# Optimization experiments

Measured on AMD Instinct MI355X. Metric: run time of the kernel, lower is better.

Reference implementation:

```python
import jax, jax.numpy as jnp
import numpy as np

B = 16; C = 20; M = 64
LEVELS = [("p3", 8, 128), ("p4", 16, 64), ("p5", 32, 32)]  # name, stride, H(=W)
BOUNDS = {"p3": (0.0, 64.0), "p4": (64.0, 128.0), "p5": (128.0, jnp.inf)}
TOPK = 1000; MAX_DET = 100; IOU_THR = 0.5; SCORE_THR = 0.3


def _grid(h, w, stride):
    # replicates get_fpn_location_coords (incl. torch's meshgrid(y, x) ordering)
    xs = stride * (jnp.arange(w, dtype=jnp.float32) + 0.5)
    ys = stride * (jnp.arange(h, dtype=jnp.float32) + 0.5)
    a, b = jnp.meshgrid(ys, xs, indexing="ij")
    return jnp.stack([a, b], axis=-1).reshape(h * w, 2)


def setup_inputs() -> dict:
    key = jax.random.key(0)
    ks = jax.random.split(key, 16)
    inp = {}
    inp["locs_p3"] = _grid(128, 128, 8)
    inp["locs_p4"] = _grid(64, 64, 16)
    inp["locs_p5"] = _grid(32, 32, 32)
    xy = jax.random.uniform(ks[0], (B, M, 2), minval=0.0, maxval=700.0)
    wh = jax.random.uniform(ks[1], (B, M, 2), minval=32.0, maxval=300.0)
    cid = jax.random.randint(ks[2], (B, M, 1), 0, C).astype(jnp.float32)
    gt = jnp.concatenate([xy, xy + wh, cid], axis=-1)
    pad = jnp.arange(M) >= (M - 16)  # last 16 rows are background padding
    inp["gt_boxes"] = jnp.where(pad[None, :, None], -1.0, gt)
    for i, (name, stride, h) in enumerate(LEVELS):
        n = h * h
        inp[f"cls_{name}"] = jax.random.normal(ks[3 + i], (B, n, C)) - 2.0
        inp[f"reg_{name}"] = jax.random.uniform(ks[6 + i], (B, n, 4), minval=0.0, maxval=8.0)
        inp[f"ctr_{name}"] = jax.random.normal(ks[9 + i], (B, n))
    return inp


def _match_level(centers, gt, lower, upper):
    # centers (N,2), gt (M,5) -> matched gt box per center (N,5), -1 for background
    x = centers[:, 0:1]; y = centers[:, 1:2]
    x0, y0, x1, y1 = gt[:, 0], gt[:, 1], gt[:, 2], gt[:, 3]
    ltrb = jnp.stack([x - x0[None], y - y0[None], x1[None] - x, y1[None] - y], axis=-1)  # (N,M,4)
    inside = ltrb.min(-1) > 0
    maxd = ltrb.max(-1)
    ok = inside & (maxd > lower) & (maxd < upper)
    areas = (x1 - x0) * (y1 - y0)
    quality = ok.astype(jnp.float32) * (1e8 - areas)[None, :]
    q = quality.max(-1)
    idx = jnp.argmax(quality, axis=-1)
    idx = jnp.where(q < 1e-5, -1, idx)
    matched = gt[jnp.clip(idx, 0)]
    return jnp.where((idx < 0)[:, None], -1.0, matched)


def _targets(centers, matched, stride):
    # fcos_get_deltas_from_locations + fcos_make_centerness_targets
    xc, yc = centers[:, 0], centers[:, 1]
    d = jnp.stack([(xc - matched[:, 0]) / stride, (yc - matched[:, 1]) / stride,
                   (matched[:, 2] - xc) / stride, (matched[:, 3] - yc) / stride], axis=1)
    bg = jnp.all(matched == -1.0, axis=1)
    d = jnp.where(bg[:, None], -1.0, d)
    l, t, r, b = d[:, 0], d[:, 1], d[:, 2], d[:, 3]
    ctr = jnp.sqrt(jnp.minimum(l, r) * jnp.minimum(t, b) / (jnp.maximum(l, r) * jnp.maximum(t, b)))
    ctr = jnp.where(jnp.all(d == -1.0, axis=1), -1.0, ctr)
    return d, ctr


def _decode(deltas, locs, stride):
    # fcos_apply_deltas_to_locations
    d = jnp.maximum(deltas, 0.0)
    xc, yc = locs[:, 0], locs[:, 1]
    return jnp.stack([xc - d[:, 0] * stride, yc - d[:, 1] * stride,
                      xc + d[:, 2] * stride, yc + d[:, 3] * stride], axis=1)


def _nms_keep(boxes, scores, valid):
    # sequential greedy NMS (argmax + IoU suppression), capped at MAX_DET picks
    areas = (boxes[:, 2] - boxes[:, 0]) * (boxes[:, 3] - boxes[:, 1])
    def body(_, state):
        active, keep = state
        s = jnp.where(active, scores, -jnp.inf)
        i = jnp.argmax(s)
        ok = s[i] > -jnp.inf
        b = boxes[i]
        xx1 = jnp.maximum(b[0], boxes[:, 0]); yy1 = jnp.maximum(b[1], boxes[:, 1])
        xx2 = jnp.minimum(b[2], boxes[:, 2]); yy2 = jnp.minimum(b[3], boxes[:, 3])
        inter = jnp.clip(xx2 - xx1, 0.0) * jnp.clip(yy2 - yy1, 0.0)
        iou = inter / (areas[i] + areas - inter)
        keep = keep.at[i].set(keep[i] | ok)
        active = jnp.where(ok, active & (iou <= IOU_THR), active)
        return active, keep
    _, keep = jax.lax.fori_loop(0, MAX_DET, body, (valid, jnp.zeros_like(valid)))
    return keep


def _infer_one(boxes, scores_cls):
    # boxes (N,4), scores_cls (N,C) -> masked detections (TOPK,5)
    score = scores_cls.max(-1)
    cls_id = jnp.argmax(scores_cls, axis=-1)
    sc, idx = jax.lax.top_k(score, TOPK)
    bx = boxes[idx]; cid = cls_id[idx]
    valid = sc > SCORE_THR
    max_coord = jnp.max(jnp.where(valid[:, None], bx, 0.0))
    off = cid.astype(bx.dtype) * (max_coord + 1.0)  # class_spec_nms offsets
    keep = _nms_keep(bx + off[:, None], sc, valid)
    det = jnp.concatenate([bx, sc[:, None]], axis=-1)
    return jnp.where(keep[:, None], det, 0.0)


def reference(locs_p3, locs_p4, locs_p5, gt_boxes, cls_p3, cls_p4, cls_p5,
              reg_p3, reg_p4, reg_p5, ctr_p3, ctr_p4, ctr_p5):
    locs = {"p3": locs_p3, "p4": locs_p4, "p5": locs_p5}
    cls = {"p3": cls_p3, "p4": cls_p4, "p5": cls_p5}
    reg = {"p3": reg_p3, "p4": reg_p4, "p5": reg_p5}
    ctr = {"p3": ctr_p3, "p4": ctr_p4, "p5": ctr_p5}
    # ---- training targets (no-grad in original) ----
    tgt_d, tgt_c = [], []
    for name, stride, _ in LEVELS:
        lo, hi = BOUNDS[name]
        matched = jax.vmap(lambda g, L=locs[name], lo=lo, hi=hi: _match_level(L, g, lo, hi))(gt_boxes)
        d, c = jax.vmap(lambda m, L=locs[name], s=stride: _targets(L, m, s))(matched)
        tgt_d.append(d); tgt_c.append(c)
    gt_deltas = jax.lax.stop_gradient(jnp.concatenate(tgt_d, axis=1))   # (B, N_total, 4)
    gt_ctr = jax.lax.stop_gradient(jnp.concatenate(tgt_c, axis=1))      # (B, N_total)
    # ---- inference: decode + score + class-specific NMS ----
    all_boxes, all_scores = [], []
    for name, stride, _ in LEVELS:
        bx = jax.vmap(lambda d, L=locs[name], s=stride: _decode(d, L, s))(reg[name])
        sc = jnp.sqrt(jax.nn.sigmoid(cls[name]) * jax.nn.sigmoid(ctr[name])[..., None])
        all_boxes.append(bx); all_scores.append(sc)
    boxes = jnp.concatenate(all_boxes, axis=1)    # (B, N_total, 4)
    scores = jnp.concatenate(all_scores, axis=1)  # (B, N_total, C)
    dets = jax.vmap(_infer_one)(boxes, scores)    # (B, TOPK, 5)
    return dets, gt_deltas, gt_ctr
```

## Files before the change

### kernel.cpp

```cpp
#include <hip/hip_runtime.h>
#include <hip/hip_bf16.h>
#include <math.h>
#include <stdint.h>

#pragma clang fp contract(off)

#define NB   16
#define NC   20
#define NM   64
#define NT   21504
#define OFF1 16384
#define OFF2 20480
#define TOPK 1000
#define DELTA_OFF 80000L
#define CTR_OFF   1456256L

__device__ __forceinline__ float ldin(const void* p, long i, int bf) {
  if (bf) return __uint_as_float(((unsigned)((const unsigned short*)p)[i]) << 16);
  return ((const float*)p)[i];
}
__device__ __forceinline__ unsigned short f2bf(float v) {
  unsigned w = __float_as_uint(v);
  return (unsigned short)((w + 0x7FFFu + ((w >> 16) & 1u)) >> 16);
}
__device__ __forceinline__ void stout(void* p, long i, float v, int bf) {
  if (bf) ((unsigned short*)p)[i] = f2bf(v);
  else    ((float*)p)[i] = v;
}

__global__ void k_flag(const void* locs0, int* flag) {
  unsigned w = ((const unsigned*)locs0)[0];
  *flag = ((w & 0xFFFFu) == 0u) ? 0 : 1;
}

__global__ __launch_bounds__(256)
void k_main(const void* locs0, const void* locs1, const void* locs2,
            const void* gt,
            const void* cls0, const void* cls1, const void* cls2,
            const void* reg0, const void* reg1, const void* reg2,
            const void* ctr0, const void* ctr1, const void* ctr2,
            void* out, float* scores, float* boxesw, float* cidw,
            const int* flagp) {
  __shared__ float sgt[NM * 5];
  __shared__ float scls[256 * 21];
  const int bf  = *flagp;
  const int b   = blockIdx.y;
  const int blk = blockIdx.x;
  const int tid = threadIdx.x;
  const int n   = blk * 256 + tid;

  const void *L, *CL, *RG, *CT; int NL, base; float stride, lower, upper;
  if (blk < 64)      { L=locs0; CL=cls0; RG=reg0; CT=ctr0; NL=16384; base=0;    stride=8.f;  lower=0.f;   upper=64.f; }
  else if (blk < 80) { L=locs1; CL=cls1; RG=reg1; CT=ctr1; NL=4096;  base=OFF1; stride=16.f; lower=64.f;  upper=128.f; }
  else               { L=locs2; CL=cls2; RG=reg2; CT=ctr2; NL=1024;  base=OFF2; stride=32.f; lower=128.f; upper=INFINITY; }
  const int nl     = n - base;
  const int nlBase = blk * 256 - base;

  for (int i = tid; i < NM * 5; i += 256) sgt[i] = ldin(gt, (long)b * NM * 5 + i, bf);

  long cbase = ((long)b * NL + nlBase) * NC;
  if (!bf) {
    const float4* p = (const float4*)((const float*)CL + cbase);
    for (int i = tid; i < 1280; i += 256) {
      float4 v = p[i];
      int e = i * 4;
      scls[( e      / 20) * 21 +  e      % 20] = v.x;
      scls[((e + 1) / 20) * 21 + (e + 1) % 20] = v.y;
      scls[((e + 2) / 20) * 21 + (e + 2) % 20] = v.z;
      scls[((e + 3) / 20) * 21 + (e + 3) % 20] = v.w;
    }
  } else {
    const unsigned* p = (const unsigned*)((const unsigned short*)CL + cbase);
    for (int i = tid; i < 2560; i += 256) {
      unsigned w = p[i];
      int e = i * 2;
      scls[( e      / 20) * 21 +  e      % 20] = __uint_as_float((w & 0xFFFFu) << 16);
      scls[((e + 1) / 20) * 21 + (e + 1) % 20] = __uint_as_float(w & 0xFFFF0000u);
    }
  }
  __syncthreads();

  float cx = ldin(L, (long)nl * 2 + 0, bf);
  float cy = ldin(L, (long)nl * 2 + 1, bf);

  float best = -1.0f; int bi = 0;
  for (int m = 0; m < NM; ++m) {
    float g0 = sgt[m*5+0], g1 = sgt[m*5+1], g2 = sgt[m*5+2], g3 = sgt[m*5+3];
    float l = cx - g0, t = cy - g1, r = g2 - cx, d = g3 - cy;
    float mn = fminf(fminf(l, t), fminf(r, d));
    float mx = fmaxf(fmaxf(l, t), fmaxf(r, d));
    bool  ok = (mn > 0.f) && (mx > lower) && (mx < upper);
    float area = (g2 - g0) * (g3 - g1);
    float q = ok ? (100000000.0f - area) : 0.f;
    if (q > best) { best = q; bi = m; }
  }
  float d0, d1, d2, d3, ctrv;
  if (best < 1e-5f) {
    d0 = d1 = d2 = d3 = -1.f; ctrv = -1.f;
  } else {
    float m0 = sgt[bi*5+0], m1 = sgt[bi*5+1], m2 = sgt[bi*5+2], m3 = sgt[bi*5+3];
    d0 = (cx - m0) / stride; d1 = (cy - m1) / stride;
    d2 = (m2 - cx) / stride; d3 = (m3 - cy) / stride;
    float mnlr = fminf(d0, d2), mntb = fminf(d1, d3);
    float mxlr = fmaxf(d0, d2), mxtb = fmaxf(d1, d3);
    ctrv = sqrtf((mnlr * mntb) / (mxlr * mxtb));
  }
  long dbase = DELTA_OFF + ((long)b * NT + n) * 4;
  if (!bf) {
    *(float4*)((float*)out + dbase) = make_float4(d0, d1, d2, d3);
  } else {
    ushort4 v; v.x = f2bf(d0); v.y = f2bf(d1); v.z = f2bf(d2); v.w = f2bf(d3);
    *(ushort4*)((unsigned short*)out + dbase) = v;
  }
  stout(out, CTR_OFF + (long)b * NT + n, ctrv, bf);

  float ct  = ldin(CT, (long)b * NL + nl, bf);
  float sct = 1.0f / (1.0f + expf(-ct));
  float smax = -1.0f; int ci = 0;
  for (int c = 0; c < NC; ++c) {
    float v  = scls[tid * 21 + c];
    float sv = 1.0f / (1.0f + expf(-v));
    float s  = sqrtf(sv * sct);
    if (s > smax) { smax = s; ci = c; }
  }
  float r0, r1, r2, r3;
  long rbase = ((long)b * NL + nl) * 4;
  if (!bf) {
    float4 rv = *(const float4*)((const float*)RG + rbase);
    r0 = rv.x; r1 = rv.y; r2 = rv.z; r3 = rv.w;
  } else {
    uint2 rw = *(const uint2*)((const unsigned short*)RG + rbase);
    r0 = __uint_as_float((rw.x & 0xFFFFu) << 16); r1 = __uint_as_float(rw.x & 0xFFFF0000u);
    r2 = __uint_as_float((rw.y & 0xFFFFu) << 16); r3 = __uint_as_float(rw.y & 0xFFFF0000u);
  }
  r0 = fmaxf(r0, 0.f); r1 = fmaxf(r1, 0.f); r2 = fmaxf(r2, 0.f); r3 = fmaxf(r3, 0.f);
  long o = (long)b * NT + n;
  scores[o] = smax;
  *(float4*)(boxesw + o * 4) =
      make_float4(cx - r0 * stride, cy - r1 * stride, cx + r2 * stride, cy + r3 * stride);
  cidw[o] = (float)ci;
}

__global__ __launch_bounds__(1024)
void k_nms(const float* scores, const float* boxesw, const float* cidw,
           void* out, const int* flagp) {
  const int bf   = *flagp;
  const int b    = blockIdx.x;
  const int tid  = threadIdx.x;
  const int wid  = tid >> 6;
  const int lane = tid & 63;
  const float* sb = scores + (long)b * NT;

  __shared__ __align__(16) char smem[49152];
  float*              sbx     = (float*)smem;
  unsigned long long* selKeys = (unsigned long long*)smem;
  float*              red     = (float*)smem;
  float*              bxs     = (float*)(smem + 20480);
  float*              scS     = (float*)(smem + 36864);
  float*              cidS    = (float*)(smem + 40960);
  float*              areaS   = (float*)(smem + 45056);
  __shared__ unsigned long long act[16];
  __shared__ unsigned long long keepMask[16];
  __shared__ unsigned wcnt_s[16];
  __shared__ unsigned selCnt;
  __shared__ int      sCurI;
  __shared__ float    sMaxC;

  unsigned inv[21];
#pragma unroll
  for (int k = 0; k < 21; ++k)
    inv[k] = ~__float_as_uint(sb[tid + k * 1024]);

  unsigned V = 0;
  for (int bit = 31; bit >= 0; --bit) {
    unsigned T = V | (1u << bit);
    unsigned c = 0;
#pragma unroll
    for (int k = 0; k < 21; ++k)
      c += (unsigned)__popcll(__ballot(inv[k] < T));
    if (lane == 0) wcnt_s[wid] = c;
    __syncthreads();
    unsigned tot = 0;
    for (int w = 0; w < 16; ++w) tot += wcnt_s[w];
    if (tot < TOPK) V = T;
    __syncthreads();
  }

  if (tid == 0) selCnt = 0u;
  __syncthreads();
#pragma unroll
  for (int k = 0; k < 21; ++k)
    if (inv[k] < V) {
      unsigned p = atomicAdd(&selCnt, 1u);
      if (p < 1024u) selKeys[p] = ((unsigned long long)inv[k] << 32) | (unsigned)(tid + k * 1024);
    }
  __syncthreads();
#pragma unroll
  for (int k = 0; k < 21; ++k)
    if (inv[k] == V) {
      unsigned p = atomicAdd(&selCnt, 1u);
      if (p < 1024u) selKeys[p] = ((unsigned long long)inv[k] << 32) | (unsigned)(tid + k * 1024);
    }
  __syncthreads();
  unsigned total = selCnt < 1024u ? selCnt : 1024u;
  if ((unsigned)tid >= total) selKeys[tid] = 0xFFFFFFFFFFFFFFFFull;
  __syncthreads();

  for (unsigned k = 2; k <= 1024; k <<= 1) {
    for (unsigned j = k >> 1; j > 0; j >>= 1) {
      unsigned ixj = (unsigned)tid ^ j;
      if (ixj > (unsigned)tid) {
        unsigned long long a = selKeys[tid], c = selKeys[ixj];
        bool up = ((tid & k) == 0);
        if (up ? (a > c) : (a < c)) { selKeys[tid] = c; selKeys[ixj] = a; }
      }
      __syncthreads();
    }
  }

  {
    unsigned long long key = selKeys[tid];
    unsigned idx  = (unsigned)key;
    unsigned kinv = (unsigned)(key >> 32);
    scS[tid] = __uint_as_float(~kinv);
    if (key != 0xFFFFFFFFFFFFFFFFull) {
      long o = (long)b * NT + idx;
      float4 bv = *(const float4*)(boxesw + o * 4);
      bxs[tid*4+0] = bv.x; bxs[tid*4+1] = bv.y; bxs[tid*4+2] = bv.z; bxs[tid*4+3] = bv.w;
      cidS[tid] = cidw[o];
    } else {
      bxs[tid*4+0] = 0.f; bxs[tid*4+1] = 0.f; bxs[tid*4+2] = 0.f; bxs[tid*4+3] = 0.f;
      cidS[tid] = 0.f;
    }
  }
  __syncthreads();

  float loc = -INFINITY;
  if (tid < TOPK)
    loc = (scS[tid] > 0.3f)
            ? fmaxf(fmaxf(bxs[tid*4+0], bxs[tid*4+1]), fmaxf(bxs[tid*4+2], bxs[tid*4+3]))
            : 0.0f;
  for (int o = 32; o > 0; o >>= 1) loc = fmaxf(loc, __shfl_down(loc, o));
  if (lane == 0) red[wid] = loc;
  __syncthreads();
  if (tid == 0) {
    float m = red[0];
    for (int w = 1; w < 16; ++w) m = fmaxf(m, red[w]);
    sMaxC = m;
  }
  __syncthreads();

  float offm = sMaxC + 1.0f;
  if (tid < TOPK) {
    float o4 = cidS[tid] * offm;
    float s0 = bxs[tid*4+0] + o4, s1 = bxs[tid*4+1] + o4;
    float s2 = bxs[tid*4+2] + o4, s3 = bxs[tid*4+3] + o4;
    sbx[tid*5+0] = s0; sbx[tid*5+1] = s1; sbx[tid*5+2] = s2; sbx[tid*5+3] = s3;
    areaS[tid] = (s2 - s0) * (s3 - s1);
  }
  bool valid = (tid < TOPK) && (scS[tid] > 0.3f);
  unsigned long long vb = __ballot(valid);
  if (lane == 0) { act[wid] = vb; keepMask[wid] = 0ull; }
  __syncthreads();

  int kept = 0;
  for (;;) {
    if (tid == 0) {
      int nxt = -1;
      for (int w = 0; w < 16; ++w) {
        unsigned long long a = act[w];
        if (a) { nxt = w * 64 + (__ffsll(a) - 1); break; }
      }
      sCurI = nxt;
    }
    __syncthreads();
    int i = sCurI;
    if (i < 0 || kept >= 100) break;
    if (tid == 0) keepMask[i >> 6] |= (1ull << (i & 63));
    float b0 = sbx[i*5+0], b1 = sbx[i*5+1], b2 = sbx[i*5+2], b3 = sbx[i*5+3];
    float ai = areaS[i];
    bool sup = false;
    if (tid < TOPK) {
      float xx1 = fmaxf(b0, sbx[tid*5+0]);
      float yy1 = fmaxf(b1, sbx[tid*5+1]);
      float xx2 = fminf(b2, sbx[tid*5+2]);
      float yy2 = fminf(b3, sbx[tid*5+3]);
      float inter = fmaxf(xx2 - xx1, 0.f) * fmaxf(yy2 - yy1, 0.f);
      float iou = inter / (ai + areaS[tid] - inter);
      sup = !(iou <= 0.5f);
    }
    unsigned long long sm = __ballot(sup);
    if (lane == 0) act[wid] &= ~sm;
    ++kept;
    __syncthreads();
  }
  __syncthreads();

  if (tid < TOPK) {
    bool kp = (keepMask[tid >> 6] >> (tid & 63)) & 1ull;
    long o = ((long)b * TOPK + tid) * 5;
    float w0 = kp ? bxs[tid*4+0] : 0.f;
    float w1 = kp ? bxs[tid*4+1] : 0.f;
    float w2 = kp ? bxs[tid*4+2] : 0.f;
    float w3 = kp ? bxs[tid*4+3] : 0.f;
    float w4 = kp ? scS[tid]     : 0.f;
    stout(out, o + 0, w0, bf); stout(out, o + 1, w1, bf);
    stout(out, o + 2, w2, bf); stout(out, o + 3, w3, bf);
    stout(out, o + 4, w4, bf);
  }
}

extern "C" void kernel_launch(void* const* d_in, const int* in_sizes, int n_in,
                              void* d_out, int out_size, void* d_ws, size_t ws_size,
                              hipStream_t stream) {
  const void* locs0 = d_in[0];
  const void* locs1 = d_in[1];
  const void* locs2 = d_in[2];
  const void* gt    = d_in[3];

  int ic[3], ir[3], it[3];
  if (n_in >= 13 && in_sizes[5] == 16 * 4096 * 20) {
    ic[0]=4; ic[1]=5; ic[2]=6;  ir[0]=7; ir[1]=8; ir[2]=9;  it[0]=10; it[1]=11; it[2]=12;
  } else {
    ic[0]=4; ic[1]=7; ic[2]=10; ir[0]=5; ir[1]=8; ir[2]=11; it[0]=6;  it[1]=9;  it[2]=12;
  }
  const void* cls0 = d_in[ic[0]]; const void* cls1 = d_in[ic[1]]; const void* cls2 = d_in[ic[2]];
  const void* reg0 = d_in[ir[0]]; const void* reg1 = d_in[ir[1]]; const void* reg2 = d_in[ir[2]];
  const void* ctr0 = d_in[it[0]]; const void* ctr1 = d_in[it[1]]; const void* ctr2 = d_in[it[2]];

  char* ws = (char*)d_ws;
  int*   flag   = (int*)ws;
  float* scores = (float*)(ws + 16);
  float* boxesw = scores + (long)NB * NT;
  float* cidw   = boxesw + (long)NB * NT * 4;

  k_flag<<<1, 1, 0, stream>>>(locs0, flag);
  k_main<<<dim3(NT / 256, NB), 256, 0, stream>>>(locs0, locs1, locs2, gt,
                                                 cls0, cls1, cls2,
                                                 reg0, reg1, reg2,
                                                 ctr0, ctr1, ctr2,
                                                 d_out, scores, boxesw, cidw, flag);
  k_nms<<<NB, 1024, 0, stream>>>(scores, boxesw, cidw, d_out, flag);
}
```

Before: 218.4 us.

## Split NMS into select, parallel IoU bitmask matrix, and single-wave greedy scan

The single per-batch NMS kernel is split into three kernels. k_select does the top-k radix select, now two bits per pass, and writes the shifted boxes. k_iou computes the full 1024x1024 suppression bitmask across many blocks. k_scan walks the greedy keep loop in one wavefront using the precomputed rows, with a double-buffered prefetch. The aim is to remove the serial loop of up to 100 block-wide barriers with per-iteration IoU, and to drop the flag-detection kernel launch. The cost is extra launches, a 4MB matrix written to and read from global memory, and IoU computed for all pairs. The matrix reuses the scores workspace region, which is safe because scores is no longer needed by then.

```diff
diff --git a/kernel.cpp b/kernel.cpp
--- a/kernel.cpp
+++ b/kernel.cpp
@@ -15,6 +15,20 @@
 #define DELTA_OFF 80000L
 #define CTR_OFF   1456256L
 
+#define WS_SCORES   0L
+#define WS_BOXESW   344064L
+#define WS_CIDW     1720320L
+#define WS_TOPSC    2064384L
+#define WS_TOPBOX   2080768L
+#define WS_TOPSHIFT 2146304L
+#define WS_TOPAREA  2211840L
+#define WS_ACT      2228224L
+#define WS_MATRIX   0L
+
+__device__ __forceinline__ int detect_bf(const void* locs0) {
+  unsigned w = *(const unsigned*)locs0;
+  return ((w & 0xFFFFu) == 0u) ? 0 : 1;
+}
 __device__ __forceinline__ float ldin(const void* p, long i, int bf) {
   if (bf) return __uint_as_float(((unsigned)((const unsigned short*)p)[i]) << 16);
   return ((const float*)p)[i];
@@ -26,11 +40,6 @@
 __device__ __forceinline__ void stout(void* p, long i, float v, int bf) {
   if (bf) ((unsigned short*)p)[i] = f2bf(v);
   else    ((float*)p)[i] = v;
-}
-
-__global__ void k_flag(const void* locs0, int* flag) {
-  unsigned w = ((const unsigned*)locs0)[0];
-  *flag = ((w & 0xFFFFu) == 0u) ? 0 : 1;
 }
 
 __global__ __launch_bounds__(256)
@@ -39,11 +48,10 @@
             const void* cls0, const void* cls1, const void* cls2,
             const void* reg0, const void* reg1, const void* reg2,
             const void* ctr0, const void* ctr1, const void* ctr2,
-            void* out, float* scores, float* boxesw, float* cidw,
-            const int* flagp) {
+            void* out, float* scores, float* boxesw, float* cidw) {
   __shared__ float sgt[NM * 5];
   __shared__ float scls[256 * 21];
-  const int bf  = *flagp;
+  const int bf  = detect_bf(locs0);
   const int b   = blockIdx.y;
   const int blk = blockIdx.x;
   const int tid = threadIdx.x;
@@ -142,47 +150,42 @@
 }
 
 __global__ __launch_bounds__(1024)
-void k_nms(const float* scores, const float* boxesw, const float* cidw,
-           void* out, const int* flagp) {
-  const int bf   = *flagp;
+void k_select(const float* scores, const float* boxesw, const float* cidw,
+              float* topScore, float* topBox, float* topShift, float* topArea,
+              unsigned long long* actInit) {
   const int b    = blockIdx.x;
   const int tid  = threadIdx.x;
   const int wid  = tid >> 6;
   const int lane = tid & 63;
   const float* sb = scores + (long)b * NT;
 
-  __shared__ __align__(16) char smem[49152];
-  float*              sbx     = (float*)smem;
-  unsigned long long* selKeys = (unsigned long long*)smem;
-  float*              red     = (float*)smem;
-  float*              bxs     = (float*)(smem + 20480);
-  float*              scS     = (float*)(smem + 36864);
-  float*              cidS    = (float*)(smem + 40960);
-  float*              areaS   = (float*)(smem + 45056);
-  __shared__ unsigned long long act[16];
-  __shared__ unsigned long long keepMask[16];
-  __shared__ unsigned wcnt_s[16];
+  __shared__ unsigned long long selKeys[1024];
+  __shared__ unsigned wcnt[16][3];
   __shared__ unsigned selCnt;
-  __shared__ int      sCurI;
-  __shared__ float    sMaxC;
+  __shared__ float redf[16];
+  __shared__ float sMaxC;
 
   unsigned inv[21];
 #pragma unroll
   for (int k = 0; k < 21; ++k)
     inv[k] = ~__float_as_uint(sb[tid + k * 1024]);
 
-  unsigned V = 0;
-  for (int bit = 31; bit >= 0; --bit) {
-    unsigned T = V | (1u << bit);
-    unsigned c = 0;
+  unsigned V = 0xC0000000u;
+  for (int s = 28; s >= 0; s -= 2) {
+    unsigned T1 = V | (1u << s), T2 = V | (2u << s), T3 = V | (3u << s);
+    unsigned c1 = 0, c2 = 0, c3 = 0;
 #pragma unroll
-    for (int k = 0; k < 21; ++k)
-      c += (unsigned)__popcll(__ballot(inv[k] < T));
-    if (lane == 0) wcnt_s[wid] = c;
+    for (int k = 0; k < 21; ++k) {
+      c1 += (unsigned)__popcll(__ballot(inv[k] < T1));
+      c2 += (unsigned)__popcll(__ballot(inv[k] < T2));
+      c3 += (unsigned)__popcll(__ballot(inv[k] < T3));
+    }
+    if (lane == 0) { wcnt[wid][0] = c1; wcnt[wid][1] = c2; wcnt[wid][2] = c3; }
     __syncthreads();
-    unsigned tot = 0;
-    for (int w = 0; w < 16; ++w) tot += wcnt_s[w];
-    if (tot < TOPK) V = T;
+    unsigned t1 = 0, t2 = 0, t3 = 0;
+    for (int w = 0; w < 16; ++w) { t1 += wcnt[w][0]; t2 += wcnt[w][1]; t3 += wcnt[w][2]; }
+    unsigned p = (t3 < TOPK) ? 3u : (t2 < TOPK) ? 2u : (t1 < TOPK) ? 1u : 0u;
+    V |= p << s;
     __syncthreads();
   }
 
@@ -218,95 +221,132 @@
     }
   }
 
-  {
-    unsigned long long key = selKeys[tid];
-    unsigned idx  = (unsigned)key;
-    unsigned kinv = (unsigned)(key >> 32);
-    scS[tid] = __uint_as_float(~kinv);
-    if (key != 0xFFFFFFFFFFFFFFFFull) {
-      long o = (long)b * NT + idx;
-      float4 bv = *(const float4*)(boxesw + o * 4);
-      bxs[tid*4+0] = bv.x; bxs[tid*4+1] = bv.y; bxs[tid*4+2] = bv.z; bxs[tid*4+3] = bv.w;
-      cidS[tid] = cidw[o];
+  unsigned long long key = selKeys[tid];
+  float sc = __uint_as_float(~(unsigned)(key >> 32));
+  float4 bv = make_float4(0.f, 0.f, 0.f, 0.f);
+  float cid = 0.f;
+  if (tid < TOPK) {
+    long o = (long)b * NT + (unsigned)key;
+    bv = *(const float4*)(boxesw + o * 4);
+    cid = cidw[o];
+  } else sc = 0.f;
+
+  float loc = (tid < TOPK)
+      ? ((sc > 0.3f) ? fmaxf(fmaxf(bv.x, bv.y), fmaxf(bv.z, bv.w)) : 0.0f)
+      : -INFINITY;
+  for (int o = 32; o > 0; o >>= 1) loc = fmaxf(loc, __shfl_down(loc, o));
+  if (lane == 0) redf[wid] = loc;
+  __syncthreads();
+  if (tid == 0) {
+    float m = redf[0];
+    for (int w = 1; w < 16; ++w) m = fmaxf(m, redf[w]);
+    sMaxC = m;
+  }
+  __syncthreads();
+
+  float offm = sMaxC + 1.0f;
+  long tb = (long)b * 1024 + tid;
+  if (tid < TOPK) {
+    float o4 = cid * offm;
+    float s0 = bv.x + o4, s1 = bv.y + o4, s2 = bv.z + o4, s3 = bv.w + o4;
+    *(float4*)(topShift + tb * 4) = make_float4(s0, s1, s2, s3);
+    topArea[tb]  = (s2 - s0) * (s3 - s1);
+    *(float4*)(topBox + tb * 4) = bv;
+    topScore[tb] = sc;
+  } else {
+    *(float4*)(topShift + tb * 4) = make_float4(0.f, 0.f, 0.f, 0.f);
+    topArea[tb]  = 0.f;
+    *(float4*)(topBox + tb * 4) = make_float4(0.f, 0.f, 0.f, 0.f);
+    topScore[tb] = 0.f;
+  }
+  unsigned long long vb = __ballot((tid < TOPK) && (sc > 0.3f));
+  if (lane == 0) actInit[b * 16 + wid] = vb;
+}
+
+__global__ __launch_bounds__(1024)
+void k_iou(const float* topShift, const float* topArea, unsigned* matrix) {
+  const int wh  = blockIdx.x;
+  const int b   = blockIdx.y;
+  const int tid = threadIdx.x;
+  const int jbase = (wh >> 1) * 64 + (wh & 1) * 32;
+  __shared__ float jx0[32], jy0[32], jx1[32], jy1[32], ja[32];
+  if (tid < 32) {
+    long tj = (long)b * 1024 + jbase + tid;
+    float4 s = *(const float4*)(topShift + tj * 4);
+    jx0[tid] = s.x; jy0[tid] = s.y; jx1[tid] = s.z; jy1[tid] = s.w;
+    ja[tid] = topArea[tj];
+  }
+  __syncthreads();
+  long ti = (long)b * 1024 + tid;
+  float4 si = *(const float4*)(topShift + ti * 4);
+  float ai  = topArea[ti];
+  unsigned word = 0u;
+  for (int k = 0; k < 32; ++k) {
+    float xx1 = fmaxf(si.x, jx0[k]);
+    float yy1 = fmaxf(si.y, jy0[k]);
+    float xx2 = fminf(si.z, jx1[k]);
+    float yy2 = fminf(si.w, jy1[k]);
+    float inter = fmaxf(xx2 - xx1, 0.f) * fmaxf(yy2 - yy1, 0.f);
+    float iou = inter / (ai + ja[k] - inter);
+    if (!(iou <= 0.5f)) word |= (1u << k);
+  }
+  matrix[ti * 32 + wh] = word;
+}
+
+__global__ __launch_bounds__(256)
+void k_scan(const unsigned long long* matrix, const unsigned long long* actInit,
+            const float* topBox, const float* topScore, void* out, const void* locs0) {
+  const int bf   = detect_bf(locs0);
+  const int b    = blockIdx.x;
+  const int tid  = threadIdx.x;
+  const int wid  = tid >> 6;
+  const int lane = tid & 63;
+  const unsigned long long* M = matrix + (long)b * 1024 * 16;
+
+  __shared__ unsigned long long rows[2][64][16];
+  __shared__ unsigned long long keepSh[16];
+
+  unsigned long long act = 0ull, keep = 0ull;
+  if (wid == 0 && lane < 16) act = actInit[b * 16 + lane];
+
+  for (int t = tid; t < 1024; t += 256)
+    rows[0][t >> 4][t & 15] = M[t];
+  __syncthreads();
+
+  int kept = 0;
+  for (int c = 0; c < 16; ++c) {
+    if (wid > 0) {
+      if (c < 15) {
+        for (int t = tid - 64; t < 1024; t += 192)
+          rows[(c + 1) & 1][t >> 4][t & 15] = M[(long)(c + 1) * 1024 + t];
+      }
     } else {
-      bxs[tid*4+0] = 0.f; bxs[tid*4+1] = 0.f; bxs[tid*4+2] = 0.f; bxs[tid*4+3] = 0.f;
-      cidS[tid] = 0.f;
-    }
-  }
-  __syncthreads();
-
-  float loc = -INFINITY;
-  if (tid < TOPK)
-    loc = (scS[tid] > 0.3f)
-            ? fmaxf(fmaxf(bxs[tid*4+0], bxs[tid*4+1]), fmaxf(bxs[tid*4+2], bxs[tid*4+3]))
-            : 0.0f;
-  for (int o = 32; o > 0; o >>= 1) loc = fmaxf(loc, __shfl_down(loc, o));
-  if (lane == 0) red[wid] = loc;
-  __syncthreads();
-  if (tid == 0) {
-    float m = red[0];
-    for (int w = 1; w < 16; ++w) m = fmaxf(m, red[w]);
-    sMaxC = m;
-  }
-  __syncthreads();
-
-  float offm = sMaxC + 1.0f;
-  if (tid < TOPK) {
-    float o4 = cidS[tid] * offm;
-    float s0 = bxs[tid*4+0] + o4, s1 = bxs[tid*4+1] + o4;
-    float s2 = bxs[tid*4+2] + o4, s3 = bxs[tid*4+3] + o4;
-    sbx[tid*5+0] = s0; sbx[tid*5+1] = s1; sbx[tid*5+2] = s2; sbx[tid*5+3] = s3;
-    areaS[tid] = (s2 - s0) * (s3 - s1);
-  }
-  bool valid = (tid < TOPK) && (scS[tid] > 0.3f);
-  unsigned long long vb = __ballot(valid);
-  if (lane == 0) { act[wid] = vb; keepMask[wid] = 0ull; }
-  __syncthreads();
-
-  int kept = 0;
-  for (;;) {
-    if (tid == 0) {
-      int nxt = -1;
-      for (int w = 0; w < 16; ++w) {
-        unsigned long long a = act[w];
-        if (a) { nxt = w * 64 + (__ffsll(a) - 1); break; }
+      unsigned long long cur = __shfl(act, c);
+      while (cur && kept < 100) {
+        int k = __ffsll((unsigned long long)cur) - 1;
+        ++kept;
+        if (lane == c) keep |= (1ull << k);
+        unsigned long long r = (lane < 16) ? rows[c & 1][k][lane] : 0ull;
+        act &= ~r;
+        cur = __shfl(act, c);
       }
-      sCurI = nxt;
     }
     __syncthreads();
-    int i = sCurI;
-    if (i < 0 || kept >= 100) break;
-    if (tid == 0) keepMask[i >> 6] |= (1ull << (i & 63));
-    float b0 = sbx[i*5+0], b1 = sbx[i*5+1], b2 = sbx[i*5+2], b3 = sbx[i*5+3];
-    float ai = areaS[i];
-    bool sup = false;
-    if (tid < TOPK) {
-      float xx1 = fmaxf(b0, sbx[tid*5+0]);
-      float yy1 = fmaxf(b1, sbx[tid*5+1]);
-      float xx2 = fminf(b2, sbx[tid*5+2]);
-      float yy2 = fminf(b3, sbx[tid*5+3]);
-      float inter = fmaxf(xx2 - xx1, 0.f) * fmaxf(yy2 - yy1, 0.f);
-      float iou = inter / (ai + areaS[tid] - inter);
-      sup = !(iou <= 0.5f);
-    }
-    unsigned long long sm = __ballot(sup);
-    if (lane == 0) act[wid] &= ~sm;
-    ++kept;
-    __syncthreads();
-  }
-  __syncthreads();
-
-  if (tid < TOPK) {
-    bool kp = (keepMask[tid >> 6] >> (tid & 63)) & 1ull;
-    long o = ((long)b * TOPK + tid) * 5;
-    float w0 = kp ? bxs[tid*4+0] : 0.f;
-    float w1 = kp ? bxs[tid*4+1] : 0.f;
-    float w2 = kp ? bxs[tid*4+2] : 0.f;
-    float w3 = kp ? bxs[tid*4+3] : 0.f;
-    float w4 = kp ? scS[tid]     : 0.f;
-    stout(out, o + 0, w0, bf); stout(out, o + 1, w1, bf);
-    stout(out, o + 2, w2, bf); stout(out, o + 3, w3, bf);
-    stout(out, o + 4, w4, bf);
+  }
+  if (wid == 0 && lane < 16) keepSh[lane] = keep;
+  __syncthreads();
+
+  for (int r = tid; r < TOPK; r += 256) {
+    bool kp = (keepSh[r >> 6] >> (r & 63)) & 1ull;
+    long tb = (long)b * 1024 + r;
+    float4 bx = *(const float4*)(topBox + tb * 4);
+    float sc  = topScore[tb];
+    long o = ((long)b * TOPK + r) * 5;
+    stout(out, o + 0, kp ? bx.x : 0.f, bf);
+    stout(out, o + 1, kp ? bx.y : 0.f, bf);
+    stout(out, o + 2, kp ? bx.z : 0.f, bf);
+    stout(out, o + 3, kp ? bx.w : 0.f, bf);
+    stout(out, o + 4, kp ? sc   : 0.f, bf);
   }
 }
 
@@ -328,17 +368,25 @@
   const void* reg0 = d_in[ir[0]]; const void* reg1 = d_in[ir[1]]; const void* reg2 = d_in[ir[2]];
   const void* ctr0 = d_in[it[0]]; const void* ctr1 = d_in[it[1]]; const void* ctr2 = d_in[it[2]];
 
-  char* ws = (char*)d_ws;
-  int*   flag   = (int*)ws;
-  float* scores = (float*)(ws + 16);
-  float* boxesw = scores + (long)NB * NT;
-  float* cidw   = boxesw + (long)NB * NT * 4;
-
-  k_flag<<<1, 1, 0, stream>>>(locs0, flag);
+  float* ws       = (float*)d_ws;
+  float* scores   = ws + WS_SCORES;
+  float* boxesw   = ws + WS_BOXESW;
+  float* cidw     = ws + WS_CIDW;
+  float* topScore = ws + WS_TOPSC;
+  float* topBox   = ws + WS_TOPBOX;
+  float* topShift = ws + WS_TOPSHIFT;
+  float* topArea  = ws + WS_TOPAREA;
+  unsigned long long* actInit = (unsigned long long*)(ws + WS_ACT);
+  unsigned*           matrix32 = (unsigned*)(ws + WS_MATRIX);
+  unsigned long long* matrix64 = (unsigned long long*)(ws + WS_MATRIX);
+
   k_main<<<dim3(NT / 256, NB), 256, 0, stream>>>(locs0, locs1, locs2, gt,
                                                  cls0, cls1, cls2,
                                                  reg0, reg1, reg2,
                                                  ctr0, ctr1, ctr2,
-                                                 d_out, scores, boxesw, cidw, flag);
-  k_nms<<<NB, 1024, 0, stream>>>(scores, boxesw, cidw, d_out, flag);
-}
+                                                 d_out, scores, boxesw, cidw);
+  k_select<<<NB, 1024, 0, stream>>>(scores, boxesw, cidw,
+                                    topScore, topBox, topShift, topArea, actInit);
+  k_iou<<<dim3(32, NB), 1024, 0, stream>>>(topShift, topArea, matrix32);
+  k_scan<<<NB, 256, 0, stream>>>(matrix64, actInit, topBox, topScore, d_out, locs0);
+}
```

Result: slower. 228.5 us (+4.7%).
